# Performance work log

Measured on AMD Instinct MI355X. Metric: run time of the kernel, lower is better.

## Reference

```python
import jax, jax.numpy as jnp
import numpy as np

C = 64
DQK = C // 8  # query/key channels


def setup_inputs() -> dict:
    key = jax.random.key(0)
    ks = jax.random.split(key, 8)
    B, H, W = 4, 64, 64
    x = jax.random.normal(ks[0], (B, C, H, W), dtype=jnp.float32)
    # 1x1 conv weights stored as (out_ch, in_ch); biases as (out_ch,)
    wq = jax.random.normal(ks[1], (DQK, C), dtype=jnp.float32) * 0.05
    bq = jnp.zeros((DQK,), dtype=jnp.float32)
    wk = jax.random.normal(ks[2], (DQK, C), dtype=jnp.float32) * 0.05
    bk = jnp.zeros((DQK,), dtype=jnp.float32)
    wv = jax.random.normal(ks[3], (C, C), dtype=jnp.float32) * 0.05
    bv = jnp.zeros((C,), dtype=jnp.float32)
    gamma = jnp.zeros((1,), dtype=jnp.float32)
    return {"x": x, "wq": wq, "bq": bq, "wk": wk, "bk": bk,
            "wv": wv, "bv": bv, "gamma": gamma}


def reference(x, wq, bq, wk, bk, wv, bv, gamma):
    B, Cc, H, W = x.shape
    N = H * W
    xf = x.reshape(B, Cc, N)  # (B, C, N)
    # 1x1 convs == channel-wise matmuls
    q = jnp.einsum('oc,bcn->bon', wq, xf) + bq[None, :, None]  # (B, dqk, N)
    k = jnp.einsum('oc,bcn->bon', wk, xf) + bk[None, :, None]  # (B, dqk, N)
    v = jnp.einsum('oc,bcn->bon', wv, xf) + bv[None, :, None]  # (B, C, N)
    # qk = q^T k -> (B, N, N), softmax over last dim
    qk = jnp.einsum('bdn,bdm->bnm', q, k)
    attn = jax.nn.softmax(qk, axis=-1)
    # out = v @ attn^T : out[b,c,i] = sum_j v[b,c,j] * attn[b,i,j]
    out = jnp.einsum('bcj,bij->bci', v, attn)
    out = out.reshape(B, Cc, H, W)
    return gamma * out + x
```

## Files before the change

kernel.cpp:

```cpp
#include <hip/hip_runtime.h>
#include <cmath>

namespace {

constexpr int B = 4;
constexpr int C = 64;
constexpr int N = 4096;
constexpr float LOG2E = 1.4426950408889634f;

typedef __bf16 bf16x8 __attribute__((ext_vector_type(8)));
typedef float f32x16 __attribute__((ext_vector_type(16)));
typedef float f32x2 __attribute__((ext_vector_type(2)));
typedef unsigned short u16;

union B8 {
  int4 i;
  bf16x8 h;
  unsigned int w[4];
};

__device__ inline u16 f2bf(float f) {
  unsigned int u = __float_as_uint(f);
  u += 0x7FFFu + ((u >> 16) & 1u);
  return (u16)(u >> 16);
}

__device__ inline unsigned int cvt_pk_bf16(float lo, float hi) {
  unsigned int r;
  asm("v_cvt_pk_bf16_f32 %0, %1, %2" : "=v"(r) : "v"(lo), "v"(hi));
  return r;
}

__device__ inline f32x2 pk_add(f32x2 a, f32x2 b) {
  f32x2 r;
  asm("v_pk_add_f32 %0, %1, %2" : "=v"(r) : "v"(a), "v"(b));
  return r;
}
__device__ inline f32x2 pk_fma(f32x2 a, f32x2 b, f32x2 c) {
  f32x2 r;
  asm("v_pk_fma_f32 %0, %1, %2, %3" : "=v"(r) : "v"(a), "v"(b), "v"(c));
  return r;
}

__device__ inline float exp2_fast(float x) {
#if __has_builtin(__builtin_amdgcn_exp2f)
  return __builtin_amdgcn_exp2f(x);
#else
  return exp2f(x);
#endif
}

__device__ __host__ inline int sigma4(int j) {
  return (j & 3) | ((j & 4) << 1) | ((j & 8) >> 1);
}

__global__ __launch_bounds__(256) void qkv_kernel(
    const float* __restrict__ x,
    const float* __restrict__ wq, const float* __restrict__ bq,
    const float* __restrict__ wk, const float* __restrict__ bk,
    const float* __restrict__ wv, const float* __restrict__ bv,
    u16* __restrict__ qt, u16* __restrict__ kt, u16* __restrict__ vo) {
  const int bid = blockIdx.x;
  const int xcd = bid & 7;
  const int b = xcd >> 1;
  const int cg = (bid >> 3) & 3;
  const int nt = (xcd & 1) * 32 + (bid >> 5);
  const int t = threadIdx.x;
  const int nn = t & 63;
  const int wid = __builtin_amdgcn_readfirstlane(t >> 6);
  const int n = nt * 64 + nn;
  const float* xb = x + (size_t)b * C * N + n;

  const int c0 = cg * 16 + wid * 4;
  f32x2 av0 = {bv[c0], 0.f}, av1 = {bv[c0 + 1], 0.f};
  f32x2 av2 = {bv[c0 + 2], 0.f}, av3 = {bv[c0 + 3], 0.f};

  if (cg == 0) {
    const int o0 = wid * 2;
    f32x2 qa0 = {bq[o0], 0.f}, qa1 = {bq[o0 + 1], 0.f};
    f32x2 ka0 = {bk[o0], 0.f}, ka1 = {bk[o0 + 1], 0.f};
    #pragma unroll 8
    for (int c = 0; c < C; c += 2) {
      const f32x2 xv = {xb[(size_t)c * N], xb[(size_t)(c + 1) * N]};
      av0 = pk_fma(*(const f32x2*)&wv[(c0 + 0) * C + c], xv, av0);
      av1 = pk_fma(*(const f32x2*)&wv[(c0 + 1) * C + c], xv, av1);
      av2 = pk_fma(*(const f32x2*)&wv[(c0 + 2) * C + c], xv, av2);
      av3 = pk_fma(*(const f32x2*)&wv[(c0 + 3) * C + c], xv, av3);
      qa0 = pk_fma(*(const f32x2*)&wq[o0 * C + c], xv, qa0);
      qa1 = pk_fma(*(const f32x2*)&wq[(o0 + 1) * C + c], xv, qa1);
      ka0 = pk_fma(*(const f32x2*)&wk[o0 * C + c], xv, ka0);
      ka1 = pk_fma(*(const f32x2*)&wk[(o0 + 1) * C + c], xv, ka1);
    }
    const unsigned int qw = (unsigned int)f2bf((qa0.x + qa0.y) * LOG2E) |
                            ((unsigned int)f2bf((qa1.x + qa1.y) * LOG2E) << 16);
    const unsigned int kw = (unsigned int)f2bf(ka0.x + ka0.y) |
                            ((unsigned int)f2bf(ka1.x + ka1.y) << 16);
    *reinterpret_cast<unsigned int*>(qt + ((size_t)b * N + n) * 8 + o0) = qw;
    *reinterpret_cast<unsigned int*>(kt + ((size_t)b * N + n) * 8 + o0) = kw;
  } else {
    #pragma unroll 8
    for (int c = 0; c < C; c += 2) {
      const f32x2 xv = {xb[(size_t)c * N], xb[(size_t)(c + 1) * N]};
      av0 = pk_fma(*(const f32x2*)&wv[(c0 + 0) * C + c], xv, av0);
      av1 = pk_fma(*(const f32x2*)&wv[(c0 + 1) * C + c], xv, av1);
      av2 = pk_fma(*(const f32x2*)&wv[(c0 + 2) * C + c], xv, av2);
      av3 = pk_fma(*(const f32x2*)&wv[(c0 + 3) * C + c], xv, av3);
    }
  }

  const int sj = sigma4(n & 15);
  const size_t tb = ((size_t)b * (N / 16) + (n >> 4)) * (C * 16) + sj;
  vo[tb + (size_t)(c0 + 0) * 16] = f2bf(av0.x + av0.y);
  vo[tb + (size_t)(c0 + 1) * 16] = f2bf(av1.x + av1.y);
  vo[tb + (size_t)(c0 + 2) * 16] = f2bf(av2.x + av2.y);
  vo[tb + (size_t)(c0 + 3) * 16] = f2bf(av3.x + av3.y);
}

__global__ __launch_bounds__(512, 4) void attn_kernel(
    const u16* __restrict__ qt, const u16* __restrict__ kt,
    const u16* __restrict__ vv, const float* __restrict__ x,
    const float* __restrict__ gamma, float* __restrict__ out) {
  const int bid = blockIdx.x;
  const int xcd = bid & 7;
  const int b = xcd >> 1;
  const int i0 = ((xcd & 1) * 64 + (bid >> 3)) * 32;
  const int t = threadIdx.x;
  const int lane = t & 63;
  const int w = __builtin_amdgcn_readfirstlane(t >> 6);
  const int il = lane & 31;
  const int hi = lane >> 5;

  __shared__ float l_lds[8][32];
  __shared__ u16 o_lds[8][32][66];

  B8 qf;
  if (hi == 0)
    qf.i = *reinterpret_cast<const int4*>(qt + ((size_t)b * N + i0 + il) * 8);
  else
    qf.i = make_int4(0, 0, 0, 0);

  const u16* kcur = kt + (size_t)b * N * 8 + ((size_t)w * 512 + il) * 8;
  const u16* vcur = vv + (size_t)b * (N / 16) * (C * 16) +
                    (size_t)w * 32 * (C * 16) + il * 16 + hi * 8;

  f32x16 accA, accB, zero16;
  #pragma unroll
  for (int r = 0; r < 16; ++r) { accA[r] = 0.f; accB[r] = 0.f; zero16[r] = 0.f; }
  f32x2 lrun2 = {0.f, 0.f};

  B8 kfA, kfB;
  B8 vaA0, vaA1;
  B8 vaB0, vaB1;

  auto BODY = [&](const B8& kf, B8& kfFree, const B8& vaC0, const B8& vaC1,
                  B8& vaN0, B8& vaN1) {
    f32x16 S = __builtin_amdgcn_mfma_f32_32x32x16_bf16(kf.h, qf.h, zero16, 0, 0, 0);
    B8 vb0, vb1;
    vb0.i = *reinterpret_cast<const int4*>(vcur + 512);
    vb1.i = *reinterpret_cast<const int4*>(vcur + 1536);
    vaN0.i = *reinterpret_cast<const int4*>(vcur + 2048);
    vaN1.i = *reinterpret_cast<const int4*>(vcur + 3072);
    kfFree.i = *reinterpret_cast<const int4*>(kcur);
    kcur += 256;
    vcur += 2048;
    float p[16];
    #pragma unroll
    for (int r = 0; r < 16; ++r) p[r] = exp2_fast(S[r]);
    B8 pf0, pf1;
    pf0.w[0] = cvt_pk_bf16(p[0], p[1]);
    pf0.w[1] = cvt_pk_bf16(p[2], p[3]);
    pf0.w[2] = cvt_pk_bf16(p[4], p[5]);
    pf0.w[3] = cvt_pk_bf16(p[6], p[7]);
    pf1.w[0] = cvt_pk_bf16(p[8], p[9]);
    pf1.w[1] = cvt_pk_bf16(p[10], p[11]);
    pf1.w[2] = cvt_pk_bf16(p[12], p[13]);
    pf1.w[3] = cvt_pk_bf16(p[14], p[15]);
    accA = __builtin_amdgcn_mfma_f32_32x32x16_bf16(vaC0.h, pf0.h, accA, 0, 0, 0);
    accA = __builtin_amdgcn_mfma_f32_32x32x16_bf16(vaC1.h, pf1.h, accA, 0, 0, 0);
    accB = __builtin_amdgcn_mfma_f32_32x32x16_bf16(vb0.h, pf0.h, accB, 0, 0, 0);
    accB = __builtin_amdgcn_mfma_f32_32x32x16_bf16(vb1.h, pf1.h, accB, 0, 0, 0);
    const f32x2* u = reinterpret_cast<const f32x2*>(p);
    f32x2 s0 = pk_add(u[0], u[1]);
    f32x2 s1 = pk_add(u[2], u[3]);
    f32x2 s2 = pk_add(u[4], u[5]);
    f32x2 s3 = pk_add(u[6], u[7]);
    s0 = pk_add(s0, s1);
    s2 = pk_add(s2, s3);
    lrun2 = pk_add(lrun2, pk_add(s0, s2));
  };

  kfA.i = *reinterpret_cast<const int4*>(kcur);
  kcur += 256;
  vaA0.i = *reinterpret_cast<const int4*>(vcur);
  vaA1.i = *reinterpret_cast<const int4*>(vcur + 1024);
  kfB.i = *reinterpret_cast<const int4*>(kcur);
  kcur += 256;

  #pragma unroll 1
  for (int it = 0; it < 8; ++it) {
    BODY(kfA, kfA, vaA0, vaA1, vaB0, vaB1);
    BODY(kfB, kfB, vaB0, vaB1, vaA0, vaA1);
  }

  const float lr = lrun2.x + lrun2.y;
  const float lw = lr + __shfl_xor(lr, 32);
  if (hi == 0) l_lds[w][il] = lw;
  #pragma unroll
  for (int r = 0; r < 16; r += 2) {
    const int c = (r & 3) + 8 * (r >> 2) + 4 * hi;
    *reinterpret_cast<unsigned int*>(&o_lds[w][il][c]) =
        cvt_pk_bf16(accA[r], accA[r + 1]);
    *reinterpret_cast<unsigned int*>(&o_lds[w][il][c + 32]) =
        cvt_pk_bf16(accB[r], accB[r + 1]);
  }
  __syncthreads();

  const int i = t & 31;
  float Li = 0.f;
  #pragma unroll
  for (int ww = 0; ww < 8; ++ww) Li += l_lds[ww][i];
  const float ginv = gamma[0] / Li;

  #pragma unroll
  for (int q4 = 0; q4 < 4; ++q4) {
    const int flat = t + q4 * 512;
    const int c = flat >> 5;
    float s = 0.f;
    #pragma unroll
    for (int ww = 0; ww < 8; ++ww)
      s += __uint_as_float((unsigned int)o_lds[ww][i][c] << 16);
    const size_t off = ((size_t)b * C + c) * N + i0 + i;
    out[off] = fmaf(ginv, s, x[off]);
  }
}

}

extern "C" void kernel_launch(void* const* d_in, const int* in_sizes, int n_in,
                              void* d_out, int out_size, void* d_ws, size_t ws_size,
                              hipStream_t stream) {
  const float* x     = (const float*)d_in[0];
  const float* wq    = (const float*)d_in[1];
  const float* bq    = (const float*)d_in[2];
  const float* wk    = (const float*)d_in[3];
  const float* bk    = (const float*)d_in[4];
  const float* wv    = (const float*)d_in[5];
  const float* bv    = (const float*)d_in[6];
  const float* gamma = (const float*)d_in[7];
  float* out = (float*)d_out;

  u16* qt = (u16*)d_ws;
  u16* kt = qt + (size_t)B * N * 8;
  u16* vo = kt + (size_t)B * N * 8;

  qkv_kernel<<<B * 64 * 4, 256, 0, stream>>>(x, wq, bq, wk, bk, wv, bv, qt, kt, vo);
  attn_kernel<<<B * (N / 32), 512, 0, stream>>>(qt, kt, vo, x, gamma, out);
}
```

Before: 29.36 us.

## Stage x tile in LDS and restructure QKV projection to 1024-thread blocks

The QKV projection kernel now uses one 1024-thread block per 64-pixel tile instead of four 256-thread blocks split by channel group. The x tile is loaded once into shared memory (transposed, padded) and reused by all 16 waves. Each wave computes 4 V channels plus one Q or K channel, which balances work that the old cg==0 branch left uneven. The change also swaps packed FMA for scalar fmaf and relaxes the attention kernel's occupancy hint from 4 to 2 blocks per CU, which may change register allocation there.

Measured after the change: 27.25 us. 7.2% less time.

```diff
diff --git a/kernel.cpp b/kernel.cpp
--- a/kernel.cpp
+++ b/kernel.cpp
@@ -34,11 +34,6 @@
 __device__ inline f32x2 pk_add(f32x2 a, f32x2 b) {
   f32x2 r;
   asm("v_pk_add_f32 %0, %1, %2" : "=v"(r) : "v"(a), "v"(b));
-  return r;
-}
-__device__ inline f32x2 pk_fma(f32x2 a, f32x2 b, f32x2 c) {
-  f32x2 r;
-  asm("v_pk_fma_f32 %0, %1, %2, %3" : "=v"(r) : "v"(a), "v"(b), "v"(c));
   return r;
 }
 
@@ -54,7 +49,7 @@
   return (j & 3) | ((j & 4) << 1) | ((j & 8) >> 1);
 }
 
-__global__ __launch_bounds__(256) void qkv_kernel(
+__global__ __launch_bounds__(1024) void qkv_kernel(
     const float* __restrict__ x,
     const float* __restrict__ wq, const float* __restrict__ bq,
     const float* __restrict__ wk, const float* __restrict__ bk,
@@ -63,60 +58,53 @@
   const int bid = blockIdx.x;
   const int xcd = bid & 7;
   const int b = xcd >> 1;
-  const int cg = (bid >> 3) & 3;
-  const int nt = (xcd & 1) * 32 + (bid >> 5);
+  const int nt = (xcd & 1) * 32 + (bid >> 3);
   const int t = threadIdx.x;
   const int nn = t & 63;
   const int wid = __builtin_amdgcn_readfirstlane(t >> 6);
-  const int n = nt * 64 + nn;
-  const float* xb = x + (size_t)b * C * N + n;
-
-  const int c0 = cg * 16 + wid * 4;
-  f32x2 av0 = {bv[c0], 0.f}, av1 = {bv[c0 + 1], 0.f};
-  f32x2 av2 = {bv[c0 + 2], 0.f}, av3 = {bv[c0 + 3], 0.f};
-
-  if (cg == 0) {
-    const int o0 = wid * 2;
-    f32x2 qa0 = {bq[o0], 0.f}, qa1 = {bq[o0 + 1], 0.f};
-    f32x2 ka0 = {bk[o0], 0.f}, ka1 = {bk[o0 + 1], 0.f};
-    #pragma unroll 8
-    for (int c = 0; c < C; c += 2) {
-      const f32x2 xv = {xb[(size_t)c * N], xb[(size_t)(c + 1) * N]};
-      av0 = pk_fma(*(const f32x2*)&wv[(c0 + 0) * C + c], xv, av0);
-      av1 = pk_fma(*(const f32x2*)&wv[(c0 + 1) * C + c], xv, av1);
-      av2 = pk_fma(*(const f32x2*)&wv[(c0 + 2) * C + c], xv, av2);
-      av3 = pk_fma(*(const f32x2*)&wv[(c0 + 3) * C + c], xv, av3);
-      qa0 = pk_fma(*(const f32x2*)&wq[o0 * C + c], xv, qa0);
-      qa1 = pk_fma(*(const f32x2*)&wq[(o0 + 1) * C + c], xv, qa1);
-      ka0 = pk_fma(*(const f32x2*)&wk[o0 * C + c], xv, ka0);
-      ka1 = pk_fma(*(const f32x2*)&wk[(o0 + 1) * C + c], xv, ka1);
-    }
-    const unsigned int qw = (unsigned int)f2bf((qa0.x + qa0.y) * LOG2E) |
-                            ((unsigned int)f2bf((qa1.x + qa1.y) * LOG2E) << 16);
-    const unsigned int kw = (unsigned int)f2bf(ka0.x + ka0.y) |
-                            ((unsigned int)f2bf(ka1.x + ka1.y) << 16);
-    *reinterpret_cast<unsigned int*>(qt + ((size_t)b * N + n) * 8 + o0) = qw;
-    *reinterpret_cast<unsigned int*>(kt + ((size_t)b * N + n) * 8 + o0) = kw;
-  } else {
-    #pragma unroll 8
-    for (int c = 0; c < C; c += 2) {
-      const f32x2 xv = {xb[(size_t)c * N], xb[(size_t)(c + 1) * N]};
-      av0 = pk_fma(*(const f32x2*)&wv[(c0 + 0) * C + c], xv, av0);
-      av1 = pk_fma(*(const f32x2*)&wv[(c0 + 1) * C + c], xv, av1);
-      av2 = pk_fma(*(const f32x2*)&wv[(c0 + 2) * C + c], xv, av2);
-      av3 = pk_fma(*(const f32x2*)&wv[(c0 + 3) * C + c], xv, av3);
-    }
-  }
+  const int n0 = nt * 64;
+  const int n = n0 + nn;
+
+  __shared__ float x_s[64][66];
+
+  const float* xb = x + (size_t)b * C * N + n0;
+  #pragma unroll
+  for (int i = 0; i < 4; ++i) {
+    const int idx = t + i * 1024;
+    const int c = idx >> 6, j = idx & 63;
+    x_s[j][c] = xb[(size_t)c * N + j];
+  }
+  __syncthreads();
+
+  const int c0 = wid * 4;
+  float a0 = bv[c0], a1 = bv[c0 + 1], a2 = bv[c0 + 2], a3 = bv[c0 + 3];
+  const float* wqk = (wid < 8) ? (wq + wid * C) : (wk + (wid - 8) * C);
+  float aqk = (wid < 8) ? bq[wid] : bk[wid - 8];
+
+  #pragma unroll 8
+  for (int c = 0; c < C; c += 2) {
+    const f32x2 xv = *reinterpret_cast<const f32x2*>(&x_s[nn][c]);
+    a0 = fmaf(wv[(c0 + 0) * C + c], xv.x, fmaf(wv[(c0 + 0) * C + c + 1], xv.y, a0));
+    a1 = fmaf(wv[(c0 + 1) * C + c], xv.x, fmaf(wv[(c0 + 1) * C + c + 1], xv.y, a1));
+    a2 = fmaf(wv[(c0 + 2) * C + c], xv.x, fmaf(wv[(c0 + 2) * C + c + 1], xv.y, a2));
+    a3 = fmaf(wv[(c0 + 3) * C + c], xv.x, fmaf(wv[(c0 + 3) * C + c + 1], xv.y, a3));
+    aqk = fmaf(wqk[c], xv.x, fmaf(wqk[c + 1], xv.y, aqk));
+  }
+
+  if (wid < 8)
+    qt[((size_t)b * N + n) * 8 + wid] = f2bf(aqk * LOG2E);
+  else
+    kt[((size_t)b * N + n) * 8 + (wid - 8)] = f2bf(aqk);
 
   const int sj = sigma4(n & 15);
   const size_t tb = ((size_t)b * (N / 16) + (n >> 4)) * (C * 16) + sj;
-  vo[tb + (size_t)(c0 + 0) * 16] = f2bf(av0.x + av0.y);
-  vo[tb + (size_t)(c0 + 1) * 16] = f2bf(av1.x + av1.y);
-  vo[tb + (size_t)(c0 + 2) * 16] = f2bf(av2.x + av2.y);
-  vo[tb + (size_t)(c0 + 3) * 16] = f2bf(av3.x + av3.y);
-}
-
-__global__ __launch_bounds__(512, 4) void attn_kernel(
+  vo[tb + (size_t)(c0 + 0) * 16] = f2bf(a0);
+  vo[tb + (size_t)(c0 + 1) * 16] = f2bf(a1);
+  vo[tb + (size_t)(c0 + 2) * 16] = f2bf(a2);
+  vo[tb + (size_t)(c0 + 3) * 16] = f2bf(a3);
+}
+
+__global__ __launch_bounds__(512, 2) void attn_kernel(
     const u16* __restrict__ qt, const u16* __restrict__ kt,
     const u16* __restrict__ vv, const float* __restrict__ x,
     const float* __restrict__ gamma, float* __restrict__ out) {
@@ -253,6 +241,6 @@
   u16* kt = qt + (size_t)B * N * 8;
   u16* vo = kt + (size_t)B * N * 8;
 
-  qkv_kernel<<<B * 64 * 4, 256, 0, stream>>>(x, wq, bq, wk, bk, wv, bv, qt, kt, vo);
+  qkv_kernel<<<B * (N / 64), 1024, 0, stream>>>(x, wq, bq, wk, bk, wv, bv, qt, kt, vo);
   attn_kernel<<<B * (N / 32), 512, 0, stream>>>(qt, kt, vo, x, gamma, out);
 }
```
